# Performance work log

Measured on AMD Instinct MI355X. Metric: run time of the kernel, lower is better.

The kernel has to match this reference:

```python
import jax, jax.numpy as jnp
import numpy as np

N = 50000      # nodes
E = 800000     # edges (before self-loops)
DIN, H1, H2, OUT = 128, 128, 64, 40
LN_EPS = 1e-5


def setup_inputs() -> dict:
    key = jax.random.key(0)
    ks = jax.random.split(key, 16)
    s = lambda d: 1.0 / np.sqrt(d)
    inp = {
        "x": jax.random.normal(ks[0], (N, DIN), jnp.float32),
        "edge_index": jax.random.randint(ks[1], (2, E), 0, N, dtype=jnp.int64),
        # GCNConv weights (applied as x @ W) and biases
        "W1": jax.random.normal(ks[2], (DIN, H1), jnp.float32) * s(DIN),
        "b1": jnp.zeros((H1,), jnp.float32),
        "W2": jax.random.normal(ks[3], (H1, H2), jnp.float32) * s(H1),
        "b2": jnp.zeros((H2,), jnp.float32),
        "W3": jax.random.normal(ks[4], (H2, H2), jnp.float32) * s(H2),
        "b3": jnp.zeros((H2,), jnp.float32),
        # LayerNorms
        "g1": jnp.ones((H1,), jnp.float32),
        "be1": jnp.zeros((H1,), jnp.float32),
        "g2": jnp.ones((H2,), jnp.float32),
        "be2": jnp.zeros((H2,), jnp.float32),
        # post_mp MLP head
        "Wp1": jax.random.normal(ks[5], (H2, H2), jnp.float32) * s(H2),
        "bp1": jnp.zeros((H2,), jnp.float32),
        "Wp2": jax.random.normal(ks[6], (H2, OUT), jnp.float32) * s(H2),
        "bp2": jnp.zeros((OUT,), jnp.float32),
    }
    return inp


def _layer_norm(x, g, b):
    mu = jnp.mean(x, axis=-1, keepdims=True)
    var = jnp.mean((x - mu) ** 2, axis=-1, keepdims=True)
    return (x - mu) * jax.lax.rsqrt(var + LN_EPS) * g + b


def _gcn(x, src, dst, norm, W, b):
    # PyG GCNConv: linear first, then normalized gather/scatter-add, bias last
    h = x @ W                                  # [N, H]
    msg = h[src] * norm[:, None]               # [E+N, H] gather
    out = jax.ops.segment_sum(msg, dst, num_segments=N)  # scatter-add
    return out + b


def reference(x, edge_index, W1, b1, W2, b2, W3, b3, g1, be1, g2, be2,
              Wp1, bp1, Wp2, bp2):
    loops = jnp.arange(N, dtype=edge_index.dtype)
    src = jnp.concatenate([edge_index[0], loops])  # add self-loops
    dst = jnp.concatenate([edge_index[1], loops])
    # symmetric normalization D^{-1/2} (A+I) D^{-1/2} (same graph all layers)
    deg = jax.ops.segment_sum(jnp.ones_like(src, dtype=x.dtype), dst,
                              num_segments=N)
    dinv = jnp.where(deg > 0, jax.lax.rsqrt(jnp.maximum(deg, 1.0)), 0.0)
    norm = dinv[src] * dinv[dst]

    h = _gcn(x, src, dst, norm, W1, b1)
    h = _layer_norm(jax.nn.relu(h), g1, be1)
    h = _gcn(h, src, dst, norm, W2, b2)
    h = _layer_norm(jax.nn.relu(h), g2, be2)
    emb = _gcn(h, src, dst, norm, W3, b3)      # emb = conv output, pre-ReLU
    h = jax.nn.relu(emb)
    h = (h @ Wp1 + bp1) @ Wp2 + bp2            # post_mp: two stacked Linears
    return emb, jax.nn.log_softmax(h, axis=1)
```

## Files before the change

### kernel.cpp

```cpp
#include <hip/hip_runtime.h>
#include <hip/hip_bf16.h>

#define DIN 128
#define HID1 128
#define HID2 64
#define OUTD 40
#define NCHUNK 64

typedef __attribute__((ext_vector_type(8))) short bf16x8;
typedef __attribute__((ext_vector_type(4))) float f32x4;

__device__ __forceinline__ float bf2f(unsigned int u) {
    union { unsigned int i; float f; } c;
    c.i = u << 16;
    return c.f;
}
__device__ __forceinline__ unsigned short f2bf(float f) {
    union { float f; unsigned int i; } c; c.f = f;
    unsigned int r = c.i + 0x7FFFu + ((c.i >> 16) & 1u);
    return (unsigned short)(r >> 16);
}
__device__ __forceinline__ unsigned int packbf(float lo, float hi) {
    return (unsigned int)f2bf(lo) | ((unsigned int)f2bf(hi) << 16);
}

__global__ void pre_kernel(const unsigned short* __restrict__ xu,
                           const int* __restrict__ ei, int* __restrict__ flags) {
    __shared__ int sh[2];
    if (threadIdx.x < 2) sh[threadIdx.x] = 0;
    __syncthreads();
    int bad = 0;
    for (int k = threadIdx.x; k < 2048; k += 256) {
        float v = bf2f(xu[2 * k]);
        float a = fabsf(v);
        if (!(a <= 1e4f) || (v != 0.f && a < 1e-4f)) bad++;
    }
    int zodd = 0;
    for (int k = threadIdx.x; k < 1024; k += 256)
        if (ei[2 * k + 1] == 0) zodd++;
    atomicAdd(&sh[0], bad);
    atomicAdd(&sh[1], zodd);
    __syncthreads();
    if (threadIdx.x == 0) {
        flags[0] = (sh[0] > 512) ? 1 : 0;
        flags[1] = (sh[1] > 512) ? 1 : 0;
    }
}

__device__ __forceinline__ int get_src(const int* ei, int E, int e, int e64) {
    return e64 ? ei[2 * e] : ei[e];
}
__device__ __forceinline__ int get_dst(const int* ei, int E, int e, int e64) {
    return e64 ? ei[2 * (E + e)] : ei[E + e];
}


__launch_bounds__(512)
__global__ void posA_kernel(const int* __restrict__ ei, int* __restrict__ pos,
                            unsigned int* __restrict__ hist, int E, int N,
                            const int* __restrict__ flags) {
    __shared__ unsigned int h32[25000];
    const int NW = (N + 1) >> 1;
    const int e64 = flags[1];
    const int b = blockIdx.x;
    const int CH = (E + NCHUNK - 1) / NCHUNK;
    const int lo = b * CH;
    int hi = lo + CH; if (hi > E) hi = E;
    for (int w = threadIdx.x; w < NW; w += 512) h32[w] = 0u;
    __syncthreads();
    for (int e = lo + threadIdx.x; e < hi; e += 512) {
        int d = get_dst(ei, E, e, e64);
        if ((unsigned)d < (unsigned)N) {
            unsigned sh = (unsigned)(d & 1) << 4;
            unsigned old = atomicAdd(&h32[d >> 1], 1u << sh);
            pos[e] = (int)((old >> sh) & 0xffffu);
        } else {
            pos[e] = -1;
        }
    }
    __syncthreads();
    unsigned int* hb = hist + (size_t)b * NW;
    for (int w = threadIdx.x; w < NW; w += 512) hb[w] = h32[w];
}

__launch_bounds__(256)
__global__ void phaseB_kernel(const unsigned int* __restrict__ hist,
                              unsigned int* __restrict__ basev,
                              int* __restrict__ cnt, int N) {
    const int NW = (N + 1) >> 1;
    const int NP = NW * 2;
    int w = blockIdx.x * 256 + threadIdx.x;
    if (w >= NW) return;
    unsigned run0 = 0, run1 = 0;
    #pragma unroll 4
    for (int b = 0; b < NCHUNK; ++b) {
        unsigned u = hist[(size_t)b * NW + w];
        uint2 bb; bb.x = run0; bb.y = run1;
        *(uint2*)&basev[(size_t)b * NP + 2 * w] = bb;
        run0 += u & 0xffffu;
        run1 += u >> 16;
    }
    cnt[2 * w] = (int)run0;
    if (2 * w + 1 < N) cnt[2 * w + 1] = (int)run1;
}


__launch_bounds__(256)
__global__ void bsum_kernel(const int* __restrict__ cnt, int* __restrict__ bsum, int N) {
    __shared__ int sh[256];
    int t = threadIdx.x;
    int i = blockIdx.x * 256 + t;
    sh[t] = (i < N) ? cnt[i] : 0;
    __syncthreads();
    #pragma unroll
    for (int off = 128; off >= 1; off >>= 1) {
        if (t < off) sh[t] += sh[t + off];
        __syncthreads();
    }
    if (t == 0) bsum[blockIdx.x] = sh[0];
}

__launch_bounds__(256)
__global__ void bscan_kernel(const int* __restrict__ bsum, int* __restrict__ bbase,
                             int* __restrict__ indptr, int NB, int N) {
    __shared__ int part[256];
    int t = threadIdx.x;
    int CH = (NB + 255) / 256;
    int lo = t * CH, hi = lo + CH; if (hi > NB) hi = NB;
    int s = 0;
    for (int i = lo; i < hi; ++i) s += bsum[i];
    part[t] = s;
    __syncthreads();
    for (int off = 1; off < 256; off <<= 1) {
        int v = (t >= off) ? part[t - off] : 0;
        __syncthreads();
        part[t] += v;
        __syncthreads();
    }
    int run = (t > 0) ? part[t - 1] : 0;
    for (int i = lo; i < hi; ++i) { bbase[i] = run; run += bsum[i]; }
    if (t == 255) indptr[N] = part[255];
}

__launch_bounds__(256)
__global__ void emit_kernel(const int* __restrict__ cnt, const int* __restrict__ bbase,
                            int* __restrict__ indptr, float* __restrict__ dinv, int N) {
    __shared__ int sh[256];
    int t = threadIdx.x;
    int i = blockIdx.x * 256 + t;
    int c = (i < N) ? cnt[i] : 0;
    sh[t] = c;
    __syncthreads();
    for (int off = 1; off < 256; off <<= 1) {
        int v = (t >= off) ? sh[t - off] : 0;
        __syncthreads();
        sh[t] += v;
        __syncthreads();
    }
    if (i < N) {
        int excl = sh[t] - c + bbase[blockIdx.x];
        indptr[i] = excl;
        dinv[i] = 1.0f / sqrtf((float)(c + 1));
    }
}

__global__ void scatter_kernel(const int* __restrict__ ei, const int* __restrict__ indptr,
                               const int* __restrict__ pos, const float* __restrict__ dinv,
                               const unsigned int* __restrict__ basev,
                               int2* __restrict__ csr_sn,
                               int E, int N, const int* __restrict__ flags) {
    int e64 = flags[1];
    int CH = (E + NCHUNK - 1) / NCHUNK;
    int NP = ((N + 1) >> 1) * 2;
    int base = (blockIdx.x * blockDim.x + threadIdx.x) * 4;
    #pragma unroll
    for (int u = 0; u < 4; ++u) {
        int e = base + u;
        if (e < E) {
            int p = pos[e];
            if (p >= 0) {
                int bb = e / CH;
                int d = get_dst(ei, E, e, e64);
                int s = get_src(ei, E, e, e64);
                if ((unsigned)s >= (unsigned)N) s = 0;
                float nrm = dinv[s] * dinv[d];
                int slot = indptr[d] + (int)basev[(size_t)bb * NP + d] + p;
                csr_sn[slot] = make_int2(s, __float_as_int(nrm));
            }
        }
    }
}


struct WCvt {
    const void* p[14];
    int sz[14];
    int off[14];
    int tobf[14];
    int cols[14];
};

__global__ void wcvt_kernel(WCvt w, unsigned short* __restrict__ wbf,
                            float* __restrict__ wf, const int* __restrict__ flags) {
    int xf32 = flags[0];
    int stride = gridDim.x * blockDim.x;
    int tid = blockIdx.x * blockDim.x + threadIdx.x;
    for (int a = 0; a < 14; ++a) {
        const float* pf = (const float*)w.p[a];
        const unsigned short* pb = (const unsigned short*)w.p[a];
        int n = w.sz[a], off = w.off[a], tobf = w.tobf[a];
        int cols = w.cols[a];
        int rows = tobf ? (n / cols) : 0;
        for (int i = tid; i < n; i += stride) {
            float v = xf32 ? pf[i] : bf2f(pb[i]);
            if (tobf) {
                int k = i / cols, m = i % cols;
                wbf[off + m * rows + k] = f2bf(v);
            } else {
                wf[off + i] = v;
            }
        }
    }
}


template<typename AT>
__device__ __forceinline__ bf16x8 ld_afrag(const AT* p);
template<>
__device__ __forceinline__ bf16x8 ld_afrag<unsigned short>(const unsigned short* p) {
    return *(const bf16x8*)p;
}
template<>
__device__ __forceinline__ bf16x8 ld_afrag<float>(const float* p) {
    float4 a = *(const float4*)p;
    float4 b = *(const float4*)(p + 4);
    bf16x8 r;
    r[0] = (short)f2bf(a.x); r[1] = (short)f2bf(a.y);
    r[2] = (short)f2bf(a.z); r[3] = (short)f2bf(a.w);
    r[4] = (short)f2bf(b.x); r[5] = (short)f2bf(b.y);
    r[6] = (short)f2bf(b.z); r[7] = (short)f2bf(b.w);
    return r;
}

template<int K, int M, typename AT>
__device__ __forceinline__ void mm_body(const AT* __restrict__ A,
                                        const unsigned short* __restrict__ WT,
                                        unsigned short* __restrict__ C, int N,
                                        unsigned short (*Ws)[K + 8]) {
    int tid = threadIdx.x;
    for (int idx = tid; idx < M * K / 8; idx += 256) {
        int r = idx / (K / 8), c8 = idx % (K / 8);
        *(uint4*)&Ws[r][c8 * 8] = *(const uint4*)&WT[r * K + c8 * 8];
    }
    __syncthreads();
    int w = tid >> 6, lane = tid & 63;
    int m = lane & 15, q = lane >> 4;
    int row_a = blockIdx.x * 64 + w * 16 + m;
    if (row_a >= N) row_a = N - 1;
    const AT* arow = A + (size_t)row_a * K;
    f32x4 acc[M / 16];
    #pragma unroll
    for (int t = 0; t < M / 16; ++t) acc[t] = (f32x4){0.f, 0.f, 0.f, 0.f};
    #pragma unroll
    for (int ks = 0; ks < K / 32; ++ks) {
        int k0 = ks * 32 + q * 8;
        bf16x8 a = ld_afrag<AT>(arow + k0);
        #pragma unroll
        for (int t = 0; t < M / 16; ++t) {
            bf16x8 b = *(const bf16x8*)&Ws[t * 16 + m][k0];
            acc[t] = __builtin_amdgcn_mfma_f32_16x16x32_bf16(a, b, acc[t], 0, 0, 0);
        }
    }
    int rbase = blockIdx.x * 64 + w * 16 + q * 4;
    #pragma unroll
    for (int reg = 0; reg < 4; ++reg) {
        int row = rbase + reg;
        if (row < N) {
            #pragma unroll
            for (int t = 0; t < M / 16; ++t)
                C[(size_t)row * M + t * 16 + m] = f2bf(acc[t][reg]);
        }
    }
}

template<int K, int M>
__launch_bounds__(256)
__global__ void mm_dual_kernel(const void* __restrict__ A,
                               const unsigned short* __restrict__ WT,
                               unsigned short* __restrict__ C, int N,
                               const int* __restrict__ flags) {
    __shared__ unsigned short Ws[M][K + 8];
    if (flags[0]) mm_body<K, M, float>((const float*)A, WT, C, N, Ws);
    else          mm_body<K, M, unsigned short>((const unsigned short*)A, WT, C, N, Ws);
}

template<int K, int M>
__launch_bounds__(256)
__global__ void mm_bf_kernel(const unsigned short* __restrict__ A,
                             const unsigned short* __restrict__ WT,
                             unsigned short* __restrict__ C, int N) {
    __shared__ unsigned short Ws[M][K + 8];
    mm_body<K, M, unsigned short>(A, WT, C, N, Ws);
}


template<int VPL>
__device__ __forceinline__ void gacc1(float* acc, const unsigned short* r, float n) {
    if constexpr (VPL == 8) {
        uint4 u = *(const uint4*)r;
        acc[0] += bf2f(u.x & 0xffffu) * n; acc[1] += bf2f(u.x >> 16) * n;
        acc[2] += bf2f(u.y & 0xffffu) * n; acc[3] += bf2f(u.y >> 16) * n;
        acc[4] += bf2f(u.z & 0xffffu) * n; acc[5] += bf2f(u.z >> 16) * n;
        acc[6] += bf2f(u.w & 0xffffu) * n; acc[7] += bf2f(u.w >> 16) * n;
    } else {
        uint2 u = *(const uint2*)r;
        acc[0] += bf2f(u.x & 0xffffu) * n; acc[1] += bf2f(u.x >> 16) * n;
        acc[2] += bf2f(u.y & 0xffffu) * n; acc[3] += bf2f(u.y >> 16) * n;
    }
}

template<int VPL>
__device__ __forceinline__ void gacc4(float* acc,
                                      const unsigned short* r0, float n0,
                                      const unsigned short* r1, float n1,
                                      const unsigned short* r2, float n2,
                                      const unsigned short* r3, float n3) {
    if constexpr (VPL == 8) {
        uint4 u0 = *(const uint4*)r0;
        uint4 u1 = *(const uint4*)r1;
        uint4 u2 = *(const uint4*)r2;
        uint4 u3 = *(const uint4*)r3;
        acc[0] += bf2f(u0.x & 0xffffu) * n0 + bf2f(u1.x & 0xffffu) * n1
                + bf2f(u2.x & 0xffffu) * n2 + bf2f(u3.x & 0xffffu) * n3;
        acc[1] += bf2f(u0.x >> 16) * n0 + bf2f(u1.x >> 16) * n1
                + bf2f(u2.x >> 16) * n2 + bf2f(u3.x >> 16) * n3;
        acc[2] += bf2f(u0.y & 0xffffu) * n0 + bf2f(u1.y & 0xffffu) * n1
                + bf2f(u2.y & 0xffffu) * n2 + bf2f(u3.y & 0xffffu) * n3;
        acc[3] += bf2f(u0.y >> 16) * n0 + bf2f(u1.y >> 16) * n1
                + bf2f(u2.y >> 16) * n2 + bf2f(u3.y >> 16) * n3;
        acc[4] += bf2f(u0.z & 0xffffu) * n0 + bf2f(u1.z & 0xffffu) * n1
                + bf2f(u2.z & 0xffffu) * n2 + bf2f(u3.z & 0xffffu) * n3;
        acc[5] += bf2f(u0.z >> 16) * n0 + bf2f(u1.z >> 16) * n1
                + bf2f(u2.z >> 16) * n2 + bf2f(u3.z >> 16) * n3;
        acc[6] += bf2f(u0.w & 0xffffu) * n0 + bf2f(u1.w & 0xffffu) * n1
                + bf2f(u2.w & 0xffffu) * n2 + bf2f(u3.w & 0xffffu) * n3;
        acc[7] += bf2f(u0.w >> 16) * n0 + bf2f(u1.w >> 16) * n1
                + bf2f(u2.w >> 16) * n2 + bf2f(u3.w >> 16) * n3;
    } else {
        uint2 u0 = *(const uint2*)r0;
        uint2 u1 = *(const uint2*)r1;
        uint2 u2 = *(const uint2*)r2;
        uint2 u3 = *(const uint2*)r3;
        acc[0] += bf2f(u0.x & 0xffffu) * n0 + bf2f(u1.x & 0xffffu) * n1
                + bf2f(u2.x & 0xffffu) * n2 + bf2f(u3.x & 0xffffu) * n3;
        acc[1] += bf2f(u0.x >> 16) * n0 + bf2f(u1.x >> 16) * n1
                + bf2f(u2.x >> 16) * n2 + bf2f(u3.x >> 16) * n3;
        acc[2] += bf2f(u0.y & 0xffffu) * n0 + bf2f(u1.y & 0xffffu) * n1
                + bf2f(u2.y & 0xffffu) * n2 + bf2f(u3.y & 0xffffu) * n3;
        acc[3] += bf2f(u0.y >> 16) * n0 + bf2f(u1.y >> 16) * n1
                + bf2f(u2.y >> 16) * n2 + bf2f(u3.y >> 16) * n3;
    }
}

template<int H, bool RELU_LN, bool EMB>
__launch_bounds__(256)
__global__ void agg_kernel(const unsigned short* __restrict__ h,
                           const int* __restrict__ indptr,
                           const int2* __restrict__ csr_sn,
                           const float* __restrict__ dinv,
                           const float* __restrict__ bias,
                           const float* __restrict__ gamma,
                           const float* __restrict__ beta,
                           unsigned short* __restrict__ out,
                           void* __restrict__ out_emb,
                           int N, const int* __restrict__ flags) {
    constexpr int VPL = H / 16;
    __shared__ int2 lsn[4][4][16];
    int w = threadIdx.x >> 6;
    int lane = threadIdx.x & 63;
    int g = lane >> 4;
    int idx = lane & 15;
    int node = blockIdx.x * 16 + w * 4 + g;
    bool active = node < N;
    int nd = active ? node : N - 1;
    float di = dinv[nd];
    int c0 = idx * VPL;
    float acc[VPL];
    #pragma unroll
    for (int v = 0; v < VPL; ++v) acc[v] = 0.f;
    gacc1<VPL>(acc, h + (size_t)nd * H + c0, di * di);
    int beg = indptr[nd], end = indptr[nd + 1];
    for (int base = beg; base < end; base += 16) {
        int m = end - base; if (m > 16) m = 16;
        if (idx < m) lsn[w][g][idx] = csr_sn[base + idx];
        int j = 0;
        for (; j + 3 < m; j += 4) {
            int2 e0 = lsn[w][g][j],     e1 = lsn[w][g][j + 1];
            int2 e2 = lsn[w][g][j + 2], e3 = lsn[w][g][j + 3];
            gacc4<VPL>(acc,
                       h + (size_t)e0.x * H + c0, __int_as_float(e0.y),
                       h + (size_t)e1.x * H + c0, __int_as_float(e1.y),
                       h + (size_t)e2.x * H + c0, __int_as_float(e2.y),
                       h + (size_t)e3.x * H + c0, __int_as_float(e3.y));
        }
        for (; j < m; ++j) {
            int2 e = lsn[w][g][j];
            gacc1<VPL>(acc, h + (size_t)e.x * H + c0, __int_as_float(e.y));
        }
    }
    #pragma unroll
    for (int v = 0; v < VPL; ++v) acc[v] += bias[c0 + v];
    if constexpr (RELU_LN) {
        #pragma unroll
        for (int v = 0; v < VPL; ++v) acc[v] = fmaxf(acc[v], 0.f);
        float s = 0.f, sq = 0.f;
        #pragma unroll
        for (int v = 0; v < VPL; ++v) { s += acc[v]; sq += acc[v] * acc[v]; }
        #pragma unroll
        for (int off = 8; off >= 1; off >>= 1) {
            s += __shfl_xor(s, off, 64);
            sq += __shfl_xor(sq, off, 64);
        }
        float mu = s * (1.0f / H);
        float var = fmaxf(sq * (1.0f / H) - mu * mu, 0.f);
        float inv = 1.0f / sqrtf(var + 1e-5f);
        #pragma unroll
        for (int v = 0; v < VPL; ++v)
            acc[v] = (acc[v] - mu) * inv * gamma[c0 + v] + beta[c0 + v];
    }
    if (active) {
        unsigned short* orow = out + (size_t)node * H + c0;
        if constexpr (VPL == 8) {
            uint4 p;
            p.x = packbf(acc[0], acc[1]); p.y = packbf(acc[2], acc[3]);
            p.z = packbf(acc[4], acc[5]); p.w = packbf(acc[6], acc[7]);
            *(uint4*)orow = p;
        } else {
            uint2 p; p.x = packbf(acc[0], acc[1]); p.y = packbf(acc[2], acc[3]);
            *(uint2*)orow = p;
        }
        if constexpr (EMB) {
            if (flags[0]) {
                float* o = (float*)out_emb + (size_t)node * H + c0;
                #pragma unroll
                for (int v4 = 0; v4 < VPL / 4; ++v4)
                    *(float4*)(o + v4 * 4) = make_float4(acc[v4 * 4], acc[v4 * 4 + 1],
                                                         acc[v4 * 4 + 2], acc[v4 * 4 + 3]);
            } else {
                unsigned short* o = (unsigned short*)out_emb + (size_t)node * H + c0;
                #pragma unroll
                for (int v2 = 0; v2 < VPL / 2; ++v2)
                    ((unsigned int*)o)[v2] = packbf(acc[v2 * 2], acc[v2 * 2 + 1]);
            }
        }
    }
}


__launch_bounds__(256)
__global__ void head_kernel(const unsigned short* __restrict__ emb,
                            const float* __restrict__ Wp1,
                            const float* __restrict__ bp1,
                            const float* __restrict__ Wp2,
                            const float* __restrict__ bp2,
                            void* __restrict__ d_out, int N,
                            const int* __restrict__ flags) {
    __shared__ float Est[64][68];
    __shared__ float W1s[64][64];
    __shared__ float Tst[64][68];
    __shared__ float W2s[64][OUTD];
    __shared__ float b1s[64];
    __shared__ float b2s[OUTD];
    int tid = threadIdx.x;
    int row0 = blockIdx.x * 64;
    for (int i = tid; i < 64 * 64; i += 256) W1s[i >> 6][i & 63] = Wp1[i];
    for (int i = tid; i < 64 * OUTD; i += 256) W2s[i / OUTD][i % OUTD] = Wp2[i];
    if (tid < 64) b1s[tid] = bp1[tid];
    if (tid < OUTD) b2s[tid] = bp2[tid];
    for (int i = tid; i < 64 * 32; i += 256) {
        int r = i >> 5, kk = i & 31;
        int row = row0 + r;
        unsigned int u = (row < N) ? *(const unsigned int*)&emb[(size_t)row * 64 + kk * 2] : 0u;
        Est[kk * 2][r]     = fmaxf(bf2f(u & 0xffffu), 0.f);
        Est[kk * 2 + 1][r] = fmaxf(bf2f(u >> 16), 0.f);
    }
    __syncthreads();
    {
        int rg = tid >> 4, cg = tid & 15;
        int r = rg * 4, c = cg * 4;
        float acc[4][4];
        #pragma unroll
        for (int i = 0; i < 4; ++i)
            #pragma unroll
            for (int jj = 0; jj < 4; ++jj) acc[i][jj] = b1s[c + jj];
        #pragma unroll 4
        for (int k = 0; k < 64; ++k) {
            float4 a = *(const float4*)&Est[k][r];
            float4 wv = *(const float4*)&W1s[k][c];
            acc[0][0] += a.x * wv.x; acc[0][1] += a.x * wv.y; acc[0][2] += a.x * wv.z; acc[0][3] += a.x * wv.w;
            acc[1][0] += a.y * wv.x; acc[1][1] += a.y * wv.y; acc[1][2] += a.y * wv.z; acc[1][3] += a.y * wv.w;
            acc[2][0] += a.z * wv.x; acc[2][1] += a.z * wv.y; acc[2][2] += a.z * wv.z; acc[2][3] += a.z * wv.w;
            acc[3][0] += a.w * wv.x; acc[3][1] += a.w * wv.y; acc[3][2] += a.w * wv.z; acc[3][3] += a.w * wv.w;
        }
        #pragma unroll
        for (int i = 0; i < 4; ++i)
            #pragma unroll
            for (int jj = 0; jj < 4; ++jj) Tst[c + jj][r + i] = acc[i][jj];
    }
    __syncthreads();
    int row = tid >> 2, tc = tid & 3, o0 = tc * 10;
    int node = row0 + row;
    float u[10];
    #pragma unroll
    for (int o = 0; o < 10; ++o) u[o] = b2s[o0 + o];
    for (int c2 = 0; c2 < 64; ++c2) {
        float tv = Tst[c2][row];
        const float2* wp = (const float2*)&W2s[c2][o0];
        #pragma unroll
        for (int o2 = 0; o2 < 5; ++o2) {
            float2 wv = wp[o2];
            u[o2 * 2]     += tv * wv.x;
            u[o2 * 2 + 1] += tv * wv.y;
        }
    }
    float mx = u[0];
    #pragma unroll
    for (int o = 1; o < 10; ++o) mx = fmaxf(mx, u[o]);
    mx = fmaxf(mx, __shfl_xor(mx, 1, 64));
    mx = fmaxf(mx, __shfl_xor(mx, 2, 64));
    float sum = 0.f;
    #pragma unroll
    for (int o = 0; o < 10; ++o) sum += __expf(u[o] - mx);
    sum += __shfl_xor(sum, 1, 64);
    sum += __shfl_xor(sum, 2, 64);
    float lse = mx + __logf(sum);
    if (node < N) {
        if (flags[0]) {
            float* base = (float*)d_out + (size_t)N * HID2;
            float* op = base + (size_t)node * OUTD + o0;
            #pragma unroll
            for (int o = 0; o < 10; ++o) op[o] = u[o] - lse;
        } else {
            unsigned short* base = (unsigned short*)d_out + (size_t)N * HID2;
            unsigned int* op = (unsigned int*)(base + (size_t)node * OUTD + o0);
            #pragma unroll
            for (int o2 = 0; o2 < 5; ++o2)
                op[o2] = packbf(u[o2 * 2] - lse, u[o2 * 2 + 1] - lse);
        }
    }
}


extern "C" void kernel_launch(void* const* d_in, const int* in_sizes, int n_in,
                              void* d_out, int out_size, void* d_ws, size_t ws_size,
                              hipStream_t stream) {
    const unsigned short* xu = (const unsigned short*)d_in[0];
    const int*            ei = (const int*)d_in[1];

    const int N = in_sizes[0] / DIN;
    const int E = in_sizes[1] / 2;
    const int NW = (N + 1) / 2;
    const int NP = NW * 2;

    size_t off = 0;
    auto take = [&](size_t bytes) {
        size_t cur = off;
        off += (bytes + 255) & ~(size_t)255;
        return cur;
    };
    char* ws = (char*)d_ws;
    int*   flags   = (int*)  (ws + take(256));
    int*   cnt     = (int*)  (ws + take((size_t)N * 4));
    float* dinv    = (float*)(ws + take((size_t)N * 4));
    int*   indptr  = (int*)  (ws + take((size_t)(N + 1) * 4));
    int*   pos     = (int*)  (ws + take((size_t)E * 4));
    int2*  csr_sn  = (int2*) (ws + take((size_t)E * 8));
    int*   bsum    = (int*)  (ws + take(((size_t)N / 256 + 2) * 4));
    int*   bbase   = (int*)  (ws + take(((size_t)N / 256 + 2) * 4));
    unsigned int* hist  = (unsigned int*)(ws + take((size_t)NCHUNK * NW * 4));
    unsigned int* basev = (unsigned int*)(ws + take((size_t)NCHUNK * NP * 4));
    unsigned short* wbf = (unsigned short*)(ws + take(32768 * 2));
    float*          wf  = (float*)         (ws + take(8192 * 4));
    unsigned short* hbuf = (unsigned short*)(ws + take((size_t)N * DIN * 2));
    unsigned short* abuf = (unsigned short*)(ws + take((size_t)N * DIN * 2));
    (void)ws_size; (void)n_in; (void)out_size;

    const int TB = 256;
    dim3 blk(TB);
    const int NB = (N + 255) / 256;

    pre_kernel<<<dim3(1), blk, 0, stream>>>(xu, ei, flags);
    posA_kernel<<<dim3(NCHUNK), dim3(512), 0, stream>>>(ei, pos, hist, E, N, flags);
    phaseB_kernel<<<dim3((NW + 255) / 256), blk, 0, stream>>>(hist, basev, cnt, N);
    bsum_kernel<<<dim3(NB), blk, 0, stream>>>(cnt, bsum, N);
    bscan_kernel<<<dim3(1), blk, 0, stream>>>(bsum, bbase, indptr, NB, N);
    emit_kernel<<<dim3(NB), blk, 0, stream>>>(cnt, bbase, indptr, dinv, N);
    scatter_kernel<<<dim3((E + 1023) / 1024), blk, 0, stream>>>(
        ei, indptr, pos, dinv, basev, csr_sn, E, N, flags);

    WCvt w;
    int bfoff = 0, foff = 0;
    int offs[14];
    const int wcols[14] = {HID1, 0, HID2, 0, HID2, 0, 0, 0, 0, 0, 0, 0, 0, 0};
    for (int a = 0; a < 14; ++a) {
        int idx = a + 2;
        w.p[a] = d_in[idx];
        w.sz[a] = in_sizes[idx];
        int tobf = (idx == 2 || idx == 4 || idx == 6) ? 1 : 0;
        w.tobf[a] = tobf;
        w.cols[a] = tobf ? wcols[a] : 1;
        if (tobf) { w.off[a] = bfoff; bfoff += in_sizes[idx]; }
        else      { w.off[a] = foff;  foff  += in_sizes[idx]; }
        offs[a] = w.off[a];
    }
    wcvt_kernel<<<dim3(64), blk, 0, stream>>>(w, wbf, wf, flags);

    unsigned short* W1t = wbf + offs[0];
    unsigned short* W2t = wbf + offs[2];
    unsigned short* W3t = wbf + offs[4];
    float* b1f  = wf + offs[1];
    float* b2f  = wf + offs[3];
    float* b3f  = wf + offs[5];
    float* g1f  = wf + offs[6];
    float* be1f = wf + offs[7];
    float* g2f  = wf + offs[8];
    float* be2f = wf + offs[9];
    float* Wp1f = wf + offs[10];
    float* bp1f = wf + offs[11];
    float* Wp2f = wf + offs[12];
    float* bp2f = wf + offs[13];

    const int MMG = (N + 63) / 64;
    const int AGG = (N + 15) / 16;

    mm_dual_kernel<DIN, HID1><<<dim3(MMG), blk, 0, stream>>>(
        d_in[0], W1t, hbuf, N, flags);
    agg_kernel<HID1, true, false><<<dim3(AGG), blk, 0, stream>>>(
        hbuf, indptr, csr_sn, dinv, b1f, g1f, be1f, abuf, nullptr, N, flags);

    mm_bf_kernel<HID1, HID2><<<dim3(MMG), blk, 0, stream>>>(abuf, W2t, hbuf, N);
    agg_kernel<HID2, true, false><<<dim3(AGG), blk, 0, stream>>>(
        hbuf, indptr, csr_sn, dinv, b2f, g2f, be2f, abuf, nullptr, N, flags);

    mm_bf_kernel<HID2, HID2><<<dim3(MMG), blk, 0, stream>>>(abuf, W3t, hbuf, N);
    agg_kernel<HID2, false, true><<<dim3(AGG), blk, 0, stream>>>(
        hbuf, indptr, csr_sn, dinv, b3f, nullptr, nullptr, abuf, d_out, N, flags);

    head_kernel<<<dim3((N + 63) / 64), blk, 0, stream>>>(
        abuf, Wp1f, bp1f, Wp2f, bp2f, d_out, N, flags);
}
```

Baseline: 306.7 us.

## Merge preprocessing kernels and split each node's edges across four lane groups

Folds the flag check, weight conversion and per-chunk histogram into one prep kernel, and folds the block-sum reduction into the phaseB prefix kernel. This removes several small launches and their serialization. The aggregation kernel now gives one wavefront per node instead of four nodes per wavefront. The 16-lane slots split the node's edge list and are combined with cross-lane shuffles, which should balance work across high-degree nodes. The cost is four times as many aggregation blocks, with three quarters of the lanes idle during the epilogue.

```diff
diff --git a/kernel.cpp b/kernel.cpp
--- a/kernel.cpp
+++ b/kernel.cpp
@@ -24,26 +24,91 @@
     return (unsigned int)f2bf(lo) | ((unsigned int)f2bf(hi) << 16);
 }
 
-__global__ void pre_kernel(const unsigned short* __restrict__ xu,
-                           const int* __restrict__ ei, int* __restrict__ flags) {
-    __shared__ int sh[2];
-    if (threadIdx.x < 2) sh[threadIdx.x] = 0;
-    __syncthreads();
-    int bad = 0;
-    for (int k = threadIdx.x; k < 2048; k += 256) {
-        float v = bf2f(xu[2 * k]);
-        float a = fabsf(v);
-        if (!(a <= 1e4f) || (v != 0.f && a < 1e-4f)) bad++;
-    }
-    int zodd = 0;
-    for (int k = threadIdx.x; k < 1024; k += 256)
-        if (ei[2 * k + 1] == 0) zodd++;
-    atomicAdd(&sh[0], bad);
-    atomicAdd(&sh[1], zodd);
-    __syncthreads();
-    if (threadIdx.x == 0) {
-        flags[0] = (sh[0] > 512) ? 1 : 0;
-        flags[1] = (sh[1] > 512) ? 1 : 0;
+struct WCvt {
+    const void* p[14];
+    int sz[14];
+    int off[14];
+    int tobf[14];
+    int cols[14];
+};
+
+
+__launch_bounds__(512)
+__global__ void prep_kernel(const unsigned short* __restrict__ xu,
+                            const int* __restrict__ ei,
+                            int* __restrict__ flags,
+                            int* __restrict__ pos,
+                            unsigned int* __restrict__ hist,
+                            WCvt wc, unsigned short* __restrict__ wbf,
+                            float* __restrict__ wf,
+                            int E, int N) {
+    __shared__ unsigned int h32[25000];
+    __shared__ int sh2[2];
+    const int NW = (N + 1) >> 1;
+    const int b = blockIdx.x;
+    const int t = threadIdx.x;
+    if (b < NCHUNK) {
+        if (t == 0) sh2[0] = 0;
+        for (int w = t; w < NW; w += 512) h32[w] = 0u;
+        __syncthreads();
+        int zodd = 0;
+        for (int k = t; k < 1024; k += 512)
+            if (ei[2 * k + 1] == 0) zodd++;
+        if (zodd) atomicAdd(&sh2[0], zodd);
+        __syncthreads();
+        const int e64 = (sh2[0] > 512) ? 1 : 0;
+        const int CH = (E + NCHUNK - 1) / NCHUNK;
+        const int lo = b * CH;
+        int hi = lo + CH; if (hi > E) hi = E;
+        for (int e = lo + t; e < hi; e += 512) {
+            int d = e64 ? ei[2 * (E + e)] : ei[E + e];
+            if ((unsigned)d < (unsigned)N) {
+                unsigned sh = (unsigned)(d & 1) << 4;
+                unsigned old = atomicAdd(&h32[d >> 1], 1u << sh);
+                pos[e] = (int)((old >> sh) & 0xffffu);
+            } else {
+                pos[e] = -1;
+            }
+        }
+        __syncthreads();
+        unsigned int* hb = hist + (size_t)b * NW;
+        for (int w = t; w < NW; w += 512) hb[w] = h32[w];
+    } else {
+        if (t < 2) sh2[t] = 0;
+        __syncthreads();
+        int bad = 0;
+        for (int k = t; k < 2048; k += 512) {
+            float v = bf2f(xu[2 * k]);
+            float a = fabsf(v);
+            if (!(a <= 1e4f) || (v != 0.f && a < 1e-4f)) bad++;
+        }
+        int zodd = 0;
+        for (int k = t; k < 1024; k += 512)
+            if (ei[2 * k + 1] == 0) zodd++;
+        if (bad) atomicAdd(&sh2[0], bad);
+        if (zodd) atomicAdd(&sh2[1], zodd);
+        __syncthreads();
+        int xf32 = (sh2[0] > 512) ? 1 : 0;
+        if (t == 0) {
+            flags[0] = xf32;
+            flags[1] = (sh2[1] > 512) ? 1 : 0;
+        }
+        for (int a = 0; a < 14; ++a) {
+            const float* pf = (const float*)wc.p[a];
+            const unsigned short* pb = (const unsigned short*)wc.p[a];
+            int n = wc.sz[a], off = wc.off[a], tobf = wc.tobf[a];
+            int cols = wc.cols[a];
+            int rows = tobf ? (n / cols) : 0;
+            for (int i = t; i < n; i += 512) {
+                float v = xf32 ? pf[i] : bf2f(pb[i]);
+                if (tobf) {
+                    int k = i / cols, m = i % cols;
+                    wbf[off + m * rows + k] = f2bf(v);
+                } else {
+                    wf[off + i] = v;
+                }
+            }
+        }
     }
 }
 
@@ -52,72 +117,42 @@
 }
 __device__ __forceinline__ int get_dst(const int* ei, int E, int e, int e64) {
     return e64 ? ei[2 * (E + e)] : ei[E + e];
-}
-
-
-__launch_bounds__(512)
-__global__ void posA_kernel(const int* __restrict__ ei, int* __restrict__ pos,
-                            unsigned int* __restrict__ hist, int E, int N,
-                            const int* __restrict__ flags) {
-    __shared__ unsigned int h32[25000];
-    const int NW = (N + 1) >> 1;
-    const int e64 = flags[1];
-    const int b = blockIdx.x;
-    const int CH = (E + NCHUNK - 1) / NCHUNK;
-    const int lo = b * CH;
-    int hi = lo + CH; if (hi > E) hi = E;
-    for (int w = threadIdx.x; w < NW; w += 512) h32[w] = 0u;
-    __syncthreads();
-    for (int e = lo + threadIdx.x; e < hi; e += 512) {
-        int d = get_dst(ei, E, e, e64);
-        if ((unsigned)d < (unsigned)N) {
-            unsigned sh = (unsigned)(d & 1) << 4;
-            unsigned old = atomicAdd(&h32[d >> 1], 1u << sh);
-            pos[e] = (int)((old >> sh) & 0xffffu);
-        } else {
-            pos[e] = -1;
-        }
-    }
-    __syncthreads();
-    unsigned int* hb = hist + (size_t)b * NW;
-    for (int w = threadIdx.x; w < NW; w += 512) hb[w] = h32[w];
 }
 
 __launch_bounds__(256)
 __global__ void phaseB_kernel(const unsigned int* __restrict__ hist,
                               unsigned int* __restrict__ basev,
-                              int* __restrict__ cnt, int N) {
+                              int* __restrict__ cnt, int* __restrict__ bsum,
+                              int N) {
+    __shared__ int red[256];
     const int NW = (N + 1) >> 1;
     const int NP = NW * 2;
-    int w = blockIdx.x * 256 + threadIdx.x;
-    if (w >= NW) return;
+    int t = threadIdx.x;
+    int w = blockIdx.x * 256 + t;
     unsigned run0 = 0, run1 = 0;
-    #pragma unroll 4
-    for (int b = 0; b < NCHUNK; ++b) {
-        unsigned u = hist[(size_t)b * NW + w];
-        uint2 bb; bb.x = run0; bb.y = run1;
-        *(uint2*)&basev[(size_t)b * NP + 2 * w] = bb;
-        run0 += u & 0xffffu;
-        run1 += u >> 16;
-    }
-    cnt[2 * w] = (int)run0;
-    if (2 * w + 1 < N) cnt[2 * w + 1] = (int)run1;
-}
-
-
-__launch_bounds__(256)
-__global__ void bsum_kernel(const int* __restrict__ cnt, int* __restrict__ bsum, int N) {
-    __shared__ int sh[256];
-    int t = threadIdx.x;
-    int i = blockIdx.x * 256 + t;
-    sh[t] = (i < N) ? cnt[i] : 0;
+    if (w < NW) {
+        #pragma unroll 4
+        for (int b = 0; b < NCHUNK; ++b) {
+            unsigned u = hist[(size_t)b * NW + w];
+            uint2 bb; bb.x = run0; bb.y = run1;
+            *(uint2*)&basev[(size_t)b * NP + 2 * w] = bb;
+            run0 += u & 0xffffu;
+            run1 += u >> 16;
+        }
+        cnt[2 * w] = (int)run0;
+        if (2 * w + 1 < N) cnt[2 * w + 1] = (int)run1;
+    }
+    int tot = 0;
+    if (w < NW) tot = (int)run0 + ((2 * w + 1 < N) ? (int)run1 : 0);
+    red[t] = tot;
     __syncthreads();
     #pragma unroll
-    for (int off = 128; off >= 1; off >>= 1) {
-        if (t < off) sh[t] += sh[t + off];
-        __syncthreads();
-    }
-    if (t == 0) bsum[blockIdx.x] = sh[0];
+    for (int off = 64; off >= 1; off >>= 1) {
+        if ((t & 127) < off) red[t] += red[t + off];
+        __syncthreads();
+    }
+    if (t == 0) bsum[2 * blockIdx.x] = red[0];
+    if (t == 128) bsum[2 * blockIdx.x + 1] = red[128];
 }
 
 __launch_bounds__(256)
@@ -186,38 +221,6 @@
                 float nrm = dinv[s] * dinv[d];
                 int slot = indptr[d] + (int)basev[(size_t)bb * NP + d] + p;
                 csr_sn[slot] = make_int2(s, __float_as_int(nrm));
-            }
-        }
-    }
-}
-
-
-struct WCvt {
-    const void* p[14];
-    int sz[14];
-    int off[14];
-    int tobf[14];
-    int cols[14];
-};
-
-__global__ void wcvt_kernel(WCvt w, unsigned short* __restrict__ wbf,
-                            float* __restrict__ wf, const int* __restrict__ flags) {
-    int xf32 = flags[0];
-    int stride = gridDim.x * blockDim.x;
-    int tid = blockIdx.x * blockDim.x + threadIdx.x;
-    for (int a = 0; a < 14; ++a) {
-        const float* pf = (const float*)w.p[a];
-        const unsigned short* pb = (const unsigned short*)w.p[a];
-        int n = w.sz[a], off = w.off[a], tobf = w.tobf[a];
-        int cols = w.cols[a];
-        int rows = tobf ? (n / cols) : 0;
-        for (int i = tid; i < n; i += stride) {
-            float v = xf32 ? pf[i] : bf2f(pb[i]);
-            if (tobf) {
-                int k = i / cols, m = i % cols;
-                wbf[off + m * rows + k] = f2bf(v);
-            } else {
-                wf[off + i] = v;
             }
         }
     }
@@ -375,12 +378,12 @@
                            void* __restrict__ out_emb,
                            int N, const int* __restrict__ flags) {
     constexpr int VPL = H / 16;
-    __shared__ int2 lsn[4][4][16];
+    __shared__ int2 lsn[4][64];
     int w = threadIdx.x >> 6;
     int lane = threadIdx.x & 63;
-    int g = lane >> 4;
+    int slot = lane >> 4;
     int idx = lane & 15;
-    int node = blockIdx.x * 16 + w * 4 + g;
+    int node = blockIdx.x * 4 + w;
     bool active = node < N;
     int nd = active ? node : N - 1;
     float di = dinv[nd];
@@ -388,25 +391,34 @@
     float acc[VPL];
     #pragma unroll
     for (int v = 0; v < VPL; ++v) acc[v] = 0.f;
-    gacc1<VPL>(acc, h + (size_t)nd * H + c0, di * di);
+    if (slot == 0)
+        gacc1<VPL>(acc, h + (size_t)nd * H + c0, di * di);
     int beg = indptr[nd], end = indptr[nd + 1];
-    for (int base = beg; base < end; base += 16) {
-        int m = end - base; if (m > 16) m = 16;
-        if (idx < m) lsn[w][g][idx] = csr_sn[base + idx];
+    for (int base = beg; base < end; base += 64) {
+        int m = end - base; if (m > 64) m = 64;
+        if (lane < m) lsn[w][lane] = csr_sn[base + lane];
+        int m16 = m & ~15;
         int j = 0;
-        for (; j + 3 < m; j += 4) {
-            int2 e0 = lsn[w][g][j],     e1 = lsn[w][g][j + 1];
-            int2 e2 = lsn[w][g][j + 2], e3 = lsn[w][g][j + 3];
+        for (; j < m16; j += 16) {
+            int2 e0 = lsn[w][j + slot];
+            int2 e1 = lsn[w][j + 4 + slot];
+            int2 e2 = lsn[w][j + 8 + slot];
+            int2 e3 = lsn[w][j + 12 + slot];
             gacc4<VPL>(acc,
                        h + (size_t)e0.x * H + c0, __int_as_float(e0.y),
                        h + (size_t)e1.x * H + c0, __int_as_float(e1.y),
                        h + (size_t)e2.x * H + c0, __int_as_float(e2.y),
                        h + (size_t)e3.x * H + c0, __int_as_float(e3.y));
         }
-        for (; j < m; ++j) {
-            int2 e = lsn[w][g][j];
+        for (int tt = j + slot; tt < m; tt += 4) {
+            int2 e = lsn[w][tt];
             gacc1<VPL>(acc, h + (size_t)e.x * H + c0, __int_as_float(e.y));
         }
+    }
+    #pragma unroll
+    for (int v = 0; v < VPL; ++v) {
+        acc[v] += __shfl_xor(acc[v], 16, 64);
+        acc[v] += __shfl_xor(acc[v], 32, 64);
     }
     #pragma unroll
     for (int v = 0; v < VPL; ++v) acc[v] += bias[c0 + v];
@@ -428,7 +440,7 @@
         for (int v = 0; v < VPL; ++v)
             acc[v] = (acc[v] - mu) * inv * gamma[c0 + v] + beta[c0 + v];
     }
-    if (active) {
+    if (active && slot == 0) {
         unsigned short* orow = out + (size_t)node * H + c0;
         if constexpr (VPL == 8) {
             uint4 p;
@@ -575,8 +587,8 @@
     int*   indptr  = (int*)  (ws + take((size_t)(N + 1) * 4));
     int*   pos     = (int*)  (ws + take((size_t)E * 4));
     int2*  csr_sn  = (int2*) (ws + take((size_t)E * 8));
-    int*   bsum    = (int*)  (ws + take(((size_t)N / 256 + 2) * 4));
-    int*   bbase   = (int*)  (ws + take(((size_t)N / 256 + 2) * 4));
+    int*   bsum    = (int*)  (ws + take(((size_t)N / 256 + 4) * 4));
+    int*   bbase   = (int*)  (ws + take(((size_t)N / 256 + 4) * 4));
     unsigned int* hist  = (unsigned int*)(ws + take((size_t)NCHUNK * NW * 4));
     unsigned int* basev = (unsigned int*)(ws + take((size_t)NCHUNK * NP * 4));
     unsigned short* wbf = (unsigned short*)(ws + take(32768 * 2));
@@ -589,31 +601,29 @@
     dim3 blk(TB);
     const int NB = (N + 255) / 256;
 
-    pre_kernel<<<dim3(1), blk, 0, stream>>>(xu, ei, flags);
-    posA_kernel<<<dim3(NCHUNK), dim3(512), 0, stream>>>(ei, pos, hist, E, N, flags);
-    phaseB_kernel<<<dim3((NW + 255) / 256), blk, 0, stream>>>(hist, basev, cnt, N);
-    bsum_kernel<<<dim3(NB), blk, 0, stream>>>(cnt, bsum, N);
-    bscan_kernel<<<dim3(1), blk, 0, stream>>>(bsum, bbase, indptr, NB, N);
-    emit_kernel<<<dim3(NB), blk, 0, stream>>>(cnt, bbase, indptr, dinv, N);
-    scatter_kernel<<<dim3((E + 1023) / 1024), blk, 0, stream>>>(
-        ei, indptr, pos, dinv, basev, csr_sn, E, N, flags);
-
-    WCvt w;
+    WCvt wc;
     int bfoff = 0, foff = 0;
     int offs[14];
     const int wcols[14] = {HID1, 0, HID2, 0, HID2, 0, 0, 0, 0, 0, 0, 0, 0, 0};
     for (int a = 0; a < 14; ++a) {
         int idx = a + 2;
-        w.p[a] = d_in[idx];
-        w.sz[a] = in_sizes[idx];
+        wc.p[a] = d_in[idx];
+        wc.sz[a] = in_sizes[idx];
         int tobf = (idx == 2 || idx == 4 || idx == 6) ? 1 : 0;
-        w.tobf[a] = tobf;
-        w.cols[a] = tobf ? wcols[a] : 1;
-        if (tobf) { w.off[a] = bfoff; bfoff += in_sizes[idx]; }
-        else      { w.off[a] = foff;  foff  += in_sizes[idx]; }
-        offs[a] = w.off[a];
-    }
-    wcvt_kernel<<<dim3(64), blk, 0, stream>>>(w, wbf, wf, flags);
+        wc.tobf[a] = tobf;
+        wc.cols[a] = tobf ? wcols[a] : 1;
+        if (tobf) { wc.off[a] = bfoff; bfoff += in_sizes[idx]; }
+        else      { wc.off[a] = foff;  foff  += in_sizes[idx]; }
+        offs[a] = wc.off[a];
+    }
+
+    prep_kernel<<<dim3(NCHUNK + 1), dim3(512), 0, stream>>>(
+        xu, ei, flags, pos, hist, wc, wbf, wf, E, N);
+    phaseB_kernel<<<dim3((NW + 255) / 256), blk, 0, stream>>>(hist, basev, cnt, bsum, N);
+    bscan_kernel<<<dim3(1), blk, 0, stream>>>(bsum, bbase, indptr, NB, N);
+    emit_kernel<<<dim3(NB), blk, 0, stream>>>(cnt, bbase, indptr, dinv, N);
+    scatter_kernel<<<dim3((E + 1023) / 1024), blk, 0, stream>>>(
+        ei, indptr, pos, dinv, basev, csr_sn, E, N, flags);
 
     unsigned short* W1t = wbf + offs[0];
     unsigned short* W2t = wbf + offs[2];
@@ -631,7 +641,7 @@
     float* bp2f = wf + offs[13];
 
     const int MMG = (N + 63) / 64;
-    const int AGG = (N + 15) / 16;
+    const int AGG = (N + 3) / 4;
 
     mm_dual_kernel<DIN, HID1><<<dim3(MMG), blk, 0, stream>>>(
         d_in[0], W1t, hbuf, N, flags);
```

Result: slower. 339.2 us (+10.6%).
